# Kernel optimization log

Hardware: AMD Instinct MI355X
Metric: run time of the kernel (lower is better)

The kernel has to match this reference:

```python
import jax, jax.numpy as jnp
import numpy as np

B, C, H, W = 4, 64, 64, 64
RATIO = 8  # channel reduction in the channel-attention branch
C8 = C // RATIO


def conv1x1(x, Wt, b):
    # 1x1 conv == channel-mixing matmul. Wt: (out_c, in_c), x: (B, in_c, H, W)
    return jnp.einsum('oc,bchw->bohw', Wt, x) + b[None, :, None, None]


def setup_inputs() -> dict:
    key = jax.random.key(0)
    ks = jax.random.split(key, 12)
    s = 0.02
    return {
        'x': jax.random.normal(ks[0], (B, C, H, W), dtype=jnp.float32),
        'y': jax.random.normal(ks[1], (B, C, H, W), dtype=jnp.float32),
        'Wq': jax.random.normal(ks[2], (C, C), dtype=jnp.float32) * s,
        'bq': jnp.zeros((C,), dtype=jnp.float32),
        'Wk': jax.random.normal(ks[3], (C, C), dtype=jnp.float32) * s,
        'bk': jnp.zeros((C,), dtype=jnp.float32),
        'Wv': jax.random.normal(ks[4], (C, C), dtype=jnp.float32) * s,
        'bv': jnp.zeros((C,), dtype=jnp.float32),
        'Wq1': jax.random.normal(ks[5], (C8, C), dtype=jnp.float32) * s,
        'bq1': jnp.zeros((C8,), dtype=jnp.float32),
        'Wk1': jax.random.normal(ks[6], (C8, C), dtype=jnp.float32) * s,
        'bk1': jnp.zeros((C8,), dtype=jnp.float32),
    }


def reference(x, y, Wq, bq, Wk, bk, Wv, bv, Wq1, bq1, Wk1, bk1):
    b, c, h, w = x.shape
    hw = h * w
    # cross-attention branch: query from y, key/value from x
    Q = conv1x1(y, Wq, bq).reshape(b, c, hw)   # (B, C, HW)
    K = conv1x1(x, Wk, bk).reshape(b, c, hw)
    V = conv1x1(x, Wv, bv).reshape(b, c, hw)
    attn = jax.nn.softmax(jnp.einsum('bcq,bck->bqk', Q, K), axis=-1)  # (B, HW, HW)
    # channel-attention branch (PAM-style spatial map from x, ratio 8)
    Q1 = conv1x1(x, Wq1, bq1).reshape(b, C8, hw)
    K1 = conv1x1(x, Wk1, bk1).reshape(b, C8, hw)
    attn1 = jax.nn.softmax(jnp.einsum('bcq,bck->bqk', Q1, K1), axis=-1)  # (B, HW, HW)
    # out = attn @ V^T + attn1 @ V^T, shape (B, HW, C)
    out = jnp.einsum('bqk,bck->bqc', attn, V) + jnp.einsum('bqk,bck->bqc', attn1, V)
    return out.transpose(0, 2, 1).reshape(b, c, h, w)
```

## Files before the change

### kernel.cpp

```cpp
#include <hip/hip_runtime.h>
#include <hip/hip_bf16.h>


typedef __bf16 bf16x8 __attribute__((ext_vector_type(8)));
typedef float f32x16 __attribute__((ext_vector_type(16)));

#define MFMA32(A, B, C) __builtin_amdgcn_mfma_f32_32x32x16_bf16((A), (B), (C), 0, 0, 0)

__device__ __forceinline__ uint4 ld16(const unsigned short* p) {
  return *reinterpret_cast<const uint4*>(p);
}
__device__ __forceinline__ bf16x8 asbf(uint4 v) {
  return __builtin_bit_cast(bf16x8, v);
}
__device__ __forceinline__ unsigned short f2bf(float f) {
  return __builtin_bit_cast(unsigned short, __float2bfloat16(f));
}
__device__ __forceinline__ unsigned pk2(float a, float b) {
  return (unsigned)f2bf(a) | ((unsigned)f2bf(b) << 16);
}

__global__ __launch_bounds__(256) void proj_kernel(
    const float* __restrict__ x, const float* __restrict__ y,
    const float* __restrict__ Wq, const float* __restrict__ bq,
    const float* __restrict__ Wk, const float* __restrict__ bk,
    const float* __restrict__ Wv, const float* __restrict__ bv,
    const float* __restrict__ Wq1, const float* __restrict__ bq1,
    const float* __restrict__ Wk1, const float* __restrict__ bk1,
    unsigned short* __restrict__ Qb, unsigned short* __restrict__ Kb,
    unsigned short* __restrict__ VtT, unsigned short* __restrict__ Q1c,
    unsigned short* __restrict__ K1c)
{
  __shared__ float ldsT[64][64];
  __shared__ float ldsW[64][65];
  __shared__ float ldsW2[64][65];
  __shared__ float ldsW1[8][64];
  __shared__ float ldsW1b[8][64];

  const int t = threadIdx.x;
  const int b = blockIdx.x >> 6;
  const int p0 = (blockIdx.x & 63) << 6;
  const int lane = t & 63;
  const int w = t >> 6;

  for (int i = t; i < 4096; i += 256) {
    int c = i >> 6, p = i & 63;
    ldsT[c][p] = y[(size_t)(b * 64 + c) * 4096 + p0 + p];
    ldsW[c][p] = Wq[i];
    ldsW2[c][p] = Wv[i];
  }
  for (int i = t; i < 512; i += 256) {
    ldsW1[i >> 6][i & 63] = Wq1[i];
    ldsW1b[i >> 6][i & 63] = Wk1[i];
  }
  __syncthreads();

  {
    float acc[16];
    float bias = bq[lane];
#pragma unroll
    for (int pp = 0; pp < 16; ++pp) acc[pp] = bias;
    for (int ic = 0; ic < 64; ++ic) {
      float wv_ = ldsW[lane][ic];
#pragma unroll
      for (int pp = 0; pp < 16; ++pp)
        acc[pp] = fmaf(wv_, ldsT[ic][w * 16 + pp], acc[pp]);
    }
#pragma unroll
    for (int pp = 0; pp < 16; ++pp)
      Qb[(size_t)(b * 4096 + p0 + w * 16 + pp) * 64 + lane] = f2bf(acc[pp]);
  }
  __syncthreads();

  for (int i = t; i < 4096; i += 256) {
    int c = i >> 6, p = i & 63;
    ldsT[c][p] = x[(size_t)(b * 64 + c) * 4096 + p0 + p];
    ldsW[c][p] = Wk[i];
  }
  __syncthreads();

  {
    float acc[16];
    float bias = bk[lane];
#pragma unroll
    for (int pp = 0; pp < 16; ++pp) acc[pp] = bias;
    for (int ic = 0; ic < 64; ++ic) {
      float wv_ = ldsW[lane][ic];
#pragma unroll
      for (int pp = 0; pp < 16; ++pp)
        acc[pp] = fmaf(wv_, ldsT[ic][w * 16 + pp], acc[pp]);
    }
#pragma unroll
    for (int pp = 0; pp < 16; ++pp)
      Kb[(size_t)(b * 4096 + p0 + w * 16 + pp) * 64 + lane] = f2bf(acc[pp]);
  }

  {
    float acc[16];
#pragma unroll
    for (int j = 0; j < 16; ++j) acc[j] = bv[16 * w + j];
    for (int ic = 0; ic < 64; ++ic) {
      float xv = ldsT[ic][lane];
#pragma unroll
      for (int j = 0; j < 16; ++j)
        acc[j] = fmaf(ldsW2[16 * w + j][ic], xv, acc[j]);
    }
    const int k = p0 + lane;
    const int kblk = k >> 5, ki = k & 31;
#pragma unroll
    for (int j = 0; j < 16; ++j)
      VtT[((size_t)(b * 128 + kblk) * 64 + 16 * w + j) * 32 + ki] = f2bf(acc[j]);
  }

  if (w == 0) {
    float acc[8];
#pragma unroll
    for (int j = 0; j < 8; ++j) acc[j] = bq1[j];
    for (int ic = 0; ic < 64; ++ic) {
      float xv = ldsT[ic][lane];
#pragma unroll
      for (int j = 0; j < 8; ++j)
        acc[j] = fmaf(ldsW1[j][ic], xv, acc[j]);
    }
    uint4 o;
    o.x = pk2(acc[0], acc[1]); o.y = pk2(acc[2], acc[3]);
    o.z = pk2(acc[4], acc[5]); o.w = pk2(acc[6], acc[7]);
    *reinterpret_cast<uint4*>(Q1c + (size_t)(b * 4096 + p0 + lane) * 8) = o;
  } else if (w == 1) {
    float acc[8];
#pragma unroll
    for (int j = 0; j < 8; ++j) acc[j] = bk1[j];
    for (int ic = 0; ic < 64; ++ic) {
      float xv = ldsT[ic][lane];
#pragma unroll
      for (int j = 0; j < 8; ++j)
        acc[j] = fmaf(ldsW1b[j][ic], xv, acc[j]);
    }
    uint4 o;
    o.x = pk2(acc[0], acc[1]); o.y = pk2(acc[2], acc[3]);
    o.z = pk2(acc[4], acc[5]); o.w = pk2(acc[6], acc[7]);
    *reinterpret_cast<uint4*>(K1c + (size_t)(b * 4096 + p0 + lane) * 8) = o;
  }
}

__global__ __launch_bounds__(256, 2) void attn_kernel(
    const unsigned short* __restrict__ Qb, const unsigned short* __restrict__ Kb,
    const unsigned short* __restrict__ VtT, const unsigned short* __restrict__ Q1c,
    const unsigned short* __restrict__ K1c, float* __restrict__ out)
{
  __shared__ float accbuf[2][2][64][32];
  __shared__ float zbuf[4][2][32];

  const int id = blockIdx.x;
  const int b = (id & 7) >> 1;
  const int qt = (id >> 3) + ((id & 1) << 6);
  const int q0 = qt * 32;

  const int wid = threadIdx.x >> 6;
  const int l = threadIdx.x & 63;
  const int qc = l & 31;
  const int h = l >> 5;

  const int kBeg = wid * 1024;
  const int kEnd = kBeg + 1024;

  const f32x16 zero16 = {0.f,0.f,0.f,0.f, 0.f,0.f,0.f,0.f,
                         0.f,0.f,0.f,0.f, 0.f,0.f,0.f,0.f};
  const uint4 zu4 = {0u, 0u, 0u, 0u};

  const unsigned short* qrow = Qb + (size_t)(b * 4096 + q0 + qc) * 64 + 8 * h;
  bf16x8 qf[4];
#pragma unroll
  for (int m = 0; m < 4; ++m) qf[m] = asbf(ld16(qrow + 16 * m));
  bf16x8 q1f;
  {
    uint4 v = zu4;
    if (h == 0) v = ld16(Q1c + (size_t)(b * 4096 + q0 + qc) * 8);
    q1f = asbf(v);
  }

  f32x16 accA0 = zero16, accA1 = zero16, accB0 = zero16, accB1 = zero16;
  float zA = 0.f, zB = 0.f;

  auto load_chunk = [&](int k0, uint4* kf, uint4& k1f, uint4* vf) {
    const unsigned short* kp = Kb + ((size_t)(b * 4096 + k0 + qc) << 6) + 8 * h;
    kf[0] = ld16(kp);
    kf[1] = ld16(kp + 16);
    kf[2] = ld16(kp + 32);
    kf[3] = ld16(kp + 48);
    k1f = zu4;
    if (h == 0) k1f = ld16(K1c + (size_t)(b * 4096 + k0 + qc) * 8);
    const unsigned short* vp =
        VtT + (((size_t)(b * 128 + (k0 >> 5)) * 64 + qc) << 5) + 8 * h;
    vf[0] = ld16(vp);
    vf[1] = ld16(vp + 16);
    vf[2] = ld16(vp + 32 * 32);
    vf[3] = ld16(vp + 32 * 32 + 16);
  };

  auto compute_chunk = [&](const uint4* kf, uint4 k1f, const uint4* vf) {
    f32x16 sD = MFMA32(asbf(kf[0]), qf[0], zero16);
    sD = MFMA32(asbf(kf[1]), qf[1], sD);
    sD = MFMA32(asbf(kf[2]), qf[2], sD);
    sD = MFMA32(asbf(kf[3]), qf[3], sD);
    f32x16 uD = MFMA32(asbf(k1f), q1f, zero16);

    float p[16], p1[16];
#pragma unroll
    for (int r = 0; r < 16; ++r) { p[r] = __expf(sD[r]); p1[r] = __expf(uD[r]); }
    zA += (((p[0]+p[1])+(p[2]+p[3])) + ((p[4]+p[5])+(p[6]+p[7]))) +
          (((p[8]+p[9])+(p[10]+p[11])) + ((p[12]+p[13])+(p[14]+p[15])));
    zB += (((p1[0]+p1[1])+(p1[2]+p1[3])) + ((p1[4]+p1[5])+(p1[6]+p1[7]))) +
          (((p1[8]+p1[9])+(p1[10]+p1[11])) + ((p1[12]+p1[13])+(p1[14]+p1[15])));

#pragma unroll
    for (int m = 0; m < 2; ++m) {
      unsigned W0 = pk2(p[8*m+0], p[8*m+1]);
      unsigned W1 = pk2(p[8*m+2], p[8*m+3]);
      unsigned W2 = pk2(p[8*m+4], p[8*m+5]);
      unsigned W3 = pk2(p[8*m+6], p[8*m+7]);
      auto s1 = __builtin_amdgcn_permlane32_swap((int)W0, (int)W2, false, false);
      auto s2 = __builtin_amdgcn_permlane32_swap((int)W1, (int)W3, false, false);
      uint4 pw;
      pw.x = (unsigned)s1[0]; pw.y = (unsigned)s2[0];
      pw.z = (unsigned)s1[1]; pw.w = (unsigned)s2[1];
      bf16x8 pf = asbf(pw);

      unsigned X0 = pk2(p1[8*m+0], p1[8*m+1]);
      unsigned X1 = pk2(p1[8*m+2], p1[8*m+3]);
      unsigned X2 = pk2(p1[8*m+4], p1[8*m+5]);
      unsigned X3 = pk2(p1[8*m+6], p1[8*m+7]);
      auto t1 = __builtin_amdgcn_permlane32_swap((int)X0, (int)X2, false, false);
      auto t2 = __builtin_amdgcn_permlane32_swap((int)X1, (int)X3, false, false);
      uint4 pw1;
      pw1.x = (unsigned)t1[0]; pw1.y = (unsigned)t2[0];
      pw1.z = (unsigned)t1[1]; pw1.w = (unsigned)t2[1];
      bf16x8 pf1 = asbf(pw1);

      accA0 = MFMA32(asbf(vf[m]),     pf,  accA0);
      accA1 = MFMA32(asbf(vf[2 + m]), pf,  accA1);
      accB0 = MFMA32(asbf(vf[m]),     pf1, accB0);
      accB1 = MFMA32(asbf(vf[2 + m]), pf1, accB1);
    }
  };

  uint4 kfA[4], vfA[4], k1fA;
  uint4 kfB[4], vfB[4], k1fB;
  load_chunk(kBeg, kfA, k1fA, vfA);
#pragma unroll 1
  for (int k0 = kBeg; k0 < kEnd; k0 += 64) {
    load_chunk(k0 + 32, kfB, k1fB, vfB);
    compute_chunk(kfA, k1fA, vfA);
    if (k0 + 64 < kEnd) load_chunk(k0 + 64, kfA, k1fA, vfA);
    compute_chunk(kfB, k1fB, vfB);
  }

  zA += __shfl_xor(zA, 32);
  zB += __shfl_xor(zB, 32);
  if (h == 0) { zbuf[wid][0][qc] = zA; zbuf[wid][1][qc] = zB; }

  auto payload_write = [&](int slot) {
#pragma unroll
    for (int r = 0; r < 16; ++r) {
      const int c0 = (r & 3) + 8 * (r >> 2) + 4 * h;
      accbuf[slot][0][c0][qc]      = accA0[r];
      accbuf[slot][0][c0 + 32][qc] = accA1[r];
      accbuf[slot][1][c0][qc]      = accB0[r];
      accbuf[slot][1][c0 + 32][qc] = accB1[r];
    }
  };
  auto payload_add = [&](int slot) {
#pragma unroll
    for (int r = 0; r < 16; ++r) {
      const int c0 = (r & 3) + 8 * (r >> 2) + 4 * h;
      accA0[r] += accbuf[slot][0][c0][qc];
      accA1[r] += accbuf[slot][0][c0 + 32][qc];
      accB0[r] += accbuf[slot][1][c0][qc];
      accB1[r] += accbuf[slot][1][c0 + 32][qc];
    }
  };

  if (wid & 1) payload_write(wid >> 1);
  __syncthreads();
  if ((wid & 1) == 0) payload_add(wid >> 1);
  __syncthreads();
  if (wid == 2) payload_write(0);
  __syncthreads();
  if (wid == 0) {
    payload_add(0);
    const float zAt = zbuf[0][0][qc] + zbuf[1][0][qc] + zbuf[2][0][qc] + zbuf[3][0][qc];
    const float zBt = zbuf[0][1][qc] + zbuf[1][1][qc] + zbuf[2][1][qc] + zbuf[3][1][qc];
    const float rA = 1.0f / zAt, rB = 1.0f / zBt;
    float* op = out + (size_t)b * (64 * 4096) + q0 + qc;
#pragma unroll
    for (int r = 0; r < 16; ++r) {
      const int c0 = (r & 3) + 8 * (r >> 2) + 4 * h;
      op[(size_t)c0 * 4096]        = accA0[r] * rA + accB0[r] * rB;
      op[(size_t)(c0 + 32) * 4096] = accA1[r] * rA + accB1[r] * rB;
    }
  }
}

extern "C" void kernel_launch(void* const* d_in, const int* in_sizes, int n_in,
                              void* d_out, int out_size, void* d_ws, size_t ws_size,
                              hipStream_t stream) {
  (void)in_sizes; (void)n_in; (void)out_size; (void)ws_size;
  const float* x = (const float*)d_in[0];
  const float* y = (const float*)d_in[1];
  const float* Wq = (const float*)d_in[2];
  const float* bq = (const float*)d_in[3];
  const float* Wk = (const float*)d_in[4];
  const float* bk = (const float*)d_in[5];
  const float* Wv = (const float*)d_in[6];
  const float* bv = (const float*)d_in[7];
  const float* Wq1 = (const float*)d_in[8];
  const float* bq1 = (const float*)d_in[9];
  const float* Wk1 = (const float*)d_in[10];
  const float* bk1 = (const float*)d_in[11];

  char* ws = (char*)d_ws;
  unsigned short* Qb = (unsigned short*)(ws);
  unsigned short* Kb = (unsigned short*)(ws + (2u << 20));
  unsigned short* VtT = (unsigned short*)(ws + (4u << 20));
  unsigned short* Q1c = (unsigned short*)(ws + (6u << 20));
  unsigned short* K1c = (unsigned short*)(ws + (6u << 20) + (256u << 10));

  proj_kernel<<<256, 256, 0, stream>>>(x, y, Wq, bq, Wk, bk, Wv, bv,
                                       Wq1, bq1, Wk1, bk1, Qb, Kb, VtT, Q1c, K1c);
  attn_kernel<<<512, 256, 0, stream>>>(Qb, Kb, VtT, Q1c, K1c, (float*)d_out);
}
```

Baseline: 77.12 us.

## Split key range across eight waves per block and use exp2 with prescaled queries

```diff
diff --git a/kernel.cpp b/kernel.cpp
--- a/kernel.cpp
+++ b/kernel.cpp
@@ -6,6 +6,9 @@
 typedef float f32x16 __attribute__((ext_vector_type(16)));
 
 #define MFMA32(A, B, C) __builtin_amdgcn_mfma_f32_32x32x16_bf16((A), (B), (C), 0, 0, 0)
+
+#define LOG2E 1.4426950408889634f
+#define EXP2F(x) __builtin_amdgcn_exp2f(x)
 
 __device__ __forceinline__ uint4 ld16(const unsigned short* p) {
   return *reinterpret_cast<const uint4*>(p);
@@ -68,7 +71,7 @@
     }
 #pragma unroll
     for (int pp = 0; pp < 16; ++pp)
-      Qb[(size_t)(b * 4096 + p0 + w * 16 + pp) * 64 + lane] = f2bf(acc[pp]);
+      Qb[(size_t)(b * 4096 + p0 + w * 16 + pp) * 64 + lane] = f2bf(acc[pp] * LOG2E);
   }
   __syncthreads();
 
@@ -123,8 +126,10 @@
         acc[j] = fmaf(ldsW1[j][ic], xv, acc[j]);
     }
     uint4 o;
-    o.x = pk2(acc[0], acc[1]); o.y = pk2(acc[2], acc[3]);
-    o.z = pk2(acc[4], acc[5]); o.w = pk2(acc[6], acc[7]);
+    o.x = pk2(acc[0] * LOG2E, acc[1] * LOG2E);
+    o.y = pk2(acc[2] * LOG2E, acc[3] * LOG2E);
+    o.z = pk2(acc[4] * LOG2E, acc[5] * LOG2E);
+    o.w = pk2(acc[6] * LOG2E, acc[7] * LOG2E);
     *reinterpret_cast<uint4*>(Q1c + (size_t)(b * 4096 + p0 + lane) * 8) = o;
   } else if (w == 1) {
     float acc[8];
@@ -143,13 +148,13 @@
   }
 }
 
-__global__ __launch_bounds__(256, 2) void attn_kernel(
+__global__ __launch_bounds__(512, 4) void attn_kernel(
     const unsigned short* __restrict__ Qb, const unsigned short* __restrict__ Kb,
     const unsigned short* __restrict__ VtT, const unsigned short* __restrict__ Q1c,
     const unsigned short* __restrict__ K1c, float* __restrict__ out)
 {
   __shared__ float accbuf[2][2][64][32];
-  __shared__ float zbuf[4][2][32];
+  __shared__ float zbuf[8][2][32];
 
   const int id = blockIdx.x;
   const int b = (id & 7) >> 1;
@@ -161,8 +166,8 @@
   const int qc = l & 31;
   const int h = l >> 5;
 
-  const int kBeg = wid * 1024;
-  const int kEnd = kBeg + 1024;
+  const int kBeg = wid << 9;
+  const int kEnd = kBeg + 512;
 
   const f32x16 zero16 = {0.f,0.f,0.f,0.f, 0.f,0.f,0.f,0.f,
                          0.f,0.f,0.f,0.f, 0.f,0.f,0.f,0.f};
@@ -207,7 +212,7 @@
 
     float p[16], p1[16];
 #pragma unroll
-    for (int r = 0; r < 16; ++r) { p[r] = __expf(sD[r]); p1[r] = __expf(uD[r]); }
+    for (int r = 0; r < 16; ++r) { p[r] = EXP2F(sD[r]); p1[r] = EXP2F(uD[r]); }
     zA += (((p[0]+p[1])+(p[2]+p[3])) + ((p[4]+p[5])+(p[6]+p[7]))) +
           (((p[8]+p[9])+(p[10]+p[11])) + ((p[12]+p[13])+(p[14]+p[15])));
     zB += (((p1[0]+p1[1])+(p1[2]+p1[3])) + ((p1[4]+p1[5])+(p1[6]+p1[7]))) +
@@ -280,16 +285,31 @@
     }
   };
 
-  if (wid & 1) payload_write(wid >> 1);
-  __syncthreads();
-  if ((wid & 1) == 0) payload_add(wid >> 1);
+  if (wid == 1) payload_write(0);
+  if (wid == 5) payload_write(1);
+  __syncthreads();
+  if (wid == 0) payload_add(0);
+  if (wid == 4) payload_add(1);
+  __syncthreads();
+  if (wid == 3) payload_write(0);
+  if (wid == 7) payload_write(1);
+  __syncthreads();
+  if (wid == 2) payload_add(0);
+  if (wid == 6) payload_add(1);
   __syncthreads();
   if (wid == 2) payload_write(0);
+  if (wid == 6) payload_write(1);
+  __syncthreads();
+  if (wid == 0) payload_add(0);
+  if (wid == 4) payload_add(1);
+  __syncthreads();
+  if (wid == 4) payload_write(0);
   __syncthreads();
   if (wid == 0) {
     payload_add(0);
-    const float zAt = zbuf[0][0][qc] + zbuf[1][0][qc] + zbuf[2][0][qc] + zbuf[3][0][qc];
-    const float zBt = zbuf[0][1][qc] + zbuf[1][1][qc] + zbuf[2][1][qc] + zbuf[3][1][qc];
+    float zAt = 0.f, zBt = 0.f;
+#pragma unroll
+    for (int ww = 0; ww < 8; ++ww) { zAt += zbuf[ww][0][qc]; zBt += zbuf[ww][1][qc]; }
     const float rA = 1.0f / zAt, rB = 1.0f / zBt;
     float* op = out + (size_t)b * (64 * 4096) + q0 + qc;
 #pragma unroll
@@ -327,5 +347,5 @@
 
   proj_kernel<<<256, 256, 0, stream>>>(x, y, Wq, bq, Wk, bk, Wv, bv,
                                        Wq1, bq1, Wk1, bk1, Qb, Kb, VtT, Q1c, K1c);
-  attn_kernel<<<512, 256, 0, stream>>>(Qb, Kb, VtT, Q1c, K1c, (float*)d_out);
-}
+  attn_kernel<<<512, 512, 0, stream>>>(Qb, Kb, VtT, Q1c, K1c, (float*)d_out);
+}
```

Measured after the change: 265.7 us. +244.6%, slower.
